# Optimization experiments

Hardware: AMD Instinct MI355X
Metric: run time of the kernel (lower is better)

## Reference

```python
import jax, jax.numpy as jnp
import numpy as np

I = 512
H = 512
B = 64
T = 512

def _lstm_step(W_ih, W_hh, b_ih, b_hh):
    def step(carry, xt):
        h, c = carry
        # gates in torch LSTMCell order: i, f, g, o
        gates = xt @ W_ih.T + b_ih + h @ W_hh.T + b_hh  # [B, 4H]
        i, f, g, o = jnp.split(gates, 4, axis=-1)
        c = jax.nn.sigmoid(f) * c + jax.nn.sigmoid(i) * jnp.tanh(g)
        h = jax.nn.sigmoid(o) * jnp.tanh(c)
        return (h, c), h
    return step

def setup_inputs() -> dict:
    key = jax.random.key(0)
    ks = jax.random.split(key, 9)
    s = 1.0 / np.sqrt(H)  # torch LSTMCell init: U(-1/sqrt(H), 1/sqrt(H))
    u = lambda k, shp: jax.random.uniform(k, shp, jnp.float32, -s, s)
    return {
        "xs": jax.random.normal(ks[0], (B, T, I), jnp.float32),
        "W_ih_f": u(ks[1], (4 * H, I)), "W_hh_f": u(ks[2], (4 * H, H)),
        "b_ih_f": u(ks[3], (4 * H,)), "b_hh_f": u(ks[4], (4 * H,)),
        "W_ih_b": u(ks[5], (4 * H, I)), "W_hh_b": u(ks[6], (4 * H, H)),
        "b_ih_b": u(ks[7], (4 * H,)), "b_hh_b": u(ks[8], (4 * H,)),
    }

def reference(xs, W_ih_f, W_hh_f, b_ih_f, b_hh_f, W_ih_b, W_hh_b, b_ih_b, b_hh_b):
    x = jnp.transpose(xs, (1, 0, 2))  # batch_first -> [T, B, I]
    b, h = x.shape[1], W_hh_f.shape[1]
    init = (jnp.zeros((b, h), x.dtype), jnp.zeros((b, h), x.dtype))
    _, hs_fwd = jax.lax.scan(_lstm_step(W_ih_f, W_hh_f, b_ih_f, b_hh_f), init, x)
    # reverse direction: scan backward, outputs land at original time indices
    _, hs_bwd = jax.lax.scan(_lstm_step(W_ih_b, W_hh_b, b_ih_b, b_hh_b), init, x, reverse=True)
    rst = jnp.concatenate([hs_fwd, hs_bwd], axis=-1)  # [T, B, 2H]
    return jnp.transpose(rst, (1, 0, 2))  # back to [B, T, 2H]
```

## Files before the change

### kernel.cpp

```cpp
#include <hip/hip_runtime.h>
#include <math.h>

#define B 64
#define T 512
#define II 512
#define H 512
#define NBLK 256

typedef float f32x4 __attribute__((ext_vector_type(4)));
typedef short s16x8 __attribute__((ext_vector_type(8)));
typedef unsigned u32;
typedef unsigned long long u64;

union pk8 { s16x8 v; u32 u[4]; };
union pk2 { u64 a[2]; uint4 q; };

__device__ __forceinline__ unsigned short f2b(float f){
  union { float f; u32 u; } v; v.f = f;
  u32 r = v.u + 0x7fffu + ((v.u >> 16) & 1u);
  return (unsigned short)(r >> 16);
}

__device__ __forceinline__ s16x8 cvt8(float4 lo, float4 hi){
  pk8 r;
  asm("v_cvt_pk_bf16_f32 %0, %1, %2" : "=v"(r.u[0]) : "v"(lo.x), "v"(lo.y));
  asm("v_cvt_pk_bf16_f32 %0, %1, %2" : "=v"(r.u[1]) : "v"(lo.z), "v"(lo.w));
  asm("v_cvt_pk_bf16_f32 %0, %1, %2" : "=v"(r.u[2]) : "v"(hi.x), "v"(hi.y));
  asm("v_cvt_pk_bf16_f32 %0, %1, %2" : "=v"(r.u[3]) : "v"(hi.z), "v"(hi.w));
  return r.v;
}

__device__ __forceinline__ float sigm_(float x){
  return __builtin_amdgcn_rcpf(1.f + __expf(-x));
}
__device__ __forceinline__ float tanh_(float x){
  float t = __expf(-2.f * fabsf(x));
  float r = (1.f - t) * __builtin_amdgcn_rcpf(1.f + t);
  return copysignf(r, x);
}

__global__ void init_ws(u32* p, int n){
  int i = blockIdx.x*blockDim.x + threadIdx.x;
  for (; i < n; i += gridDim.x*blockDim.x) p[i] = 0u;
}

__global__ __launch_bounds__(256, 1) void lstm_persistent(
    const float* __restrict__ xs,
    const float* __restrict__ Wih_f, const float* __restrict__ Whh_f,
    const float* __restrict__ bih_f, const float* __restrict__ bhh_f,
    const float* __restrict__ Wih_b, const float* __restrict__ Whh_b,
    const float* __restrict__ bih_b, const float* __restrict__ bhh_b,
    float* __restrict__ out,
    u32* __restrict__ flags,
    u32* __restrict__ hbuf0, u32* __restrict__ hbuf1)
{
  __shared__ unsigned short Wlds[4*16*1024];
  __shared__ unsigned short Hlds[16*512];
  __shared__ float g_lds[4][16][16];
  __shared__ float bias_s[64];

  const int tid = threadIdx.x;
  const int bx = blockIdx.x;
  const int dir   = bx >> 7;
  const int qtile = bx & 31;
  const int btile = (bx >> 5) & 3;
  const int grp   = bx >> 5;
  const int q0 = qtile * 16;
  const int b0 = btile * 16;

  const float* __restrict__ Wih = dir ? Wih_b : Wih_f;
  const float* __restrict__ Whh = dir ? Whh_b : Whh_f;
  const float* __restrict__ bih = dir ? bih_b : bih_f;
  const float* __restrict__ bhh = dir ? bhh_b : bhh_f;

  for (int it = 0; it < 32; ++it){
    int idx = it * 256 + tid;
    int c64 = idx >> 7;
    int k   = (idx & 127) * 8;
    int cg  = (c64 >> 4) * H + q0 + (c64 & 15);
    const float* src = (k < II) ? (Wih + (size_t)cg * II + k)
                                : (Whh + (size_t)cg * H + (k - II));
    float4 lo = *(const float4*)src;
    float4 hi = *(const float4*)(src + 4);
    s16x8 v;
    v[0]=(short)f2b(lo.x); v[1]=(short)f2b(lo.y); v[2]=(short)f2b(lo.z); v[3]=(short)f2b(lo.w);
    v[4]=(short)f2b(hi.x); v[5]=(short)f2b(hi.y); v[6]=(short)f2b(hi.z); v[7]=(short)f2b(hi.w);
    u32 byte = ((u32)c64 * 2048u + (u32)k * 2u) ^ (((u32)(c64 & 7)) << 4);
    *(s16x8*)((char*)Wlds + byte) = v;
  }
  if (tid < 64){
    int g = tid >> 4, jj = tid & 15;
    int cg = g * H + q0 + jj;
    bias_s[tid] = bih[cg] + bhh[cg];
  }
  __syncthreads();

  const int w = tid >> 6;
  const int l = tid & 63;
  const int arow = b0 + (l & 15);
  const int kgrp = (l >> 4) * 8;
  const int c64w = (w << 4) | (l & 15);
  const u32 swz   = ((u32)(c64w & 7)) << 4;
  const u32 wbase = (u32)c64w * 2048u;
  const u32 hrb = (u32)(l & 15) * 1024u;
  const u32 hsz = ((u32)(l & 7)) << 4;

  const int sr = w * 4;
  const int si = l;

  const int eb = tid >> 4;
  const int ej = tid & 15;
  float c_reg = 0.f;

  const size_t hdir = (size_t)dir * (B * (H/2));
  u32* const fl = flags + grp * 32;

  s16x8 a_x[16];
  {
    const int t0 = dir ? (T-1) : 0;
    const float* xrow = xs + ((size_t)arow * T + t0) * II + kgrp;
    #pragma unroll
    for (int ks = 0; ks < 16; ++ks)
      a_x[ks] = cvt8(*(const float4*)(xrow + ks*32), *(const float4*)(xrow + ks*32 + 4));
  }

  #pragma unroll 1
  for (int s = 0; s < T; ++s){
    const int t = dir ? (T - 1 - s) : s;
    const u32* __restrict__ hin  = (s & 1) ? hbuf1 : hbuf0;
    u32* __restrict__       hout = (s & 1) ? hbuf0 : hbuf1;

    if (s > 0){
      for (;;){
        u32 v = __hip_atomic_load(&fl[si & 31], __ATOMIC_RELAXED, __HIP_MEMORY_SCOPE_AGENT);
        if (__all((int)(v >= (u32)s))) break;
      }
    }

    u64 hv[8];
    #pragma unroll
    for (int p = 0; p < 4; ++p){
      const u64* src = (const u64*)(hin + hdir + (size_t)(b0 + sr + p) * (H/2)) + (size_t)si * 2;
      hv[2*p+0] = __hip_atomic_load(src + 0, __ATOMIC_RELAXED, __HIP_MEMORY_SCOPE_AGENT);
      hv[2*p+1] = __hip_atomic_load(src + 1, __ATOMIC_RELAXED, __HIP_MEMORY_SCOPE_AGENT);
    }

    f32x4 acc_xa = {0.f,0.f,0.f,0.f}, acc_xb = {0.f,0.f,0.f,0.f};
    #pragma unroll
    for (int ks = 0; ks < 8; ++ks){
      u32 byte0 = (wbase + (u32)(ks*32 + kgrp) * 2u) ^ swz;
      u32 byte1 = (wbase + (u32)((ks+8)*32 + kgrp) * 2u) ^ swz;
      s16x8 b0f = *(const s16x8*)((const char*)Wlds + byte0);
      s16x8 b1f = *(const s16x8*)((const char*)Wlds + byte1);
      acc_xa = __builtin_amdgcn_mfma_f32_16x16x32_bf16(a_x[ks],   b0f, acc_xa, 0, 0, 0);
      acc_xb = __builtin_amdgcn_mfma_f32_16x16x32_bf16(a_x[ks+8], b1f, acc_xb, 0, 0, 0);
    }

    #pragma unroll
    for (int p = 0; p < 4; ++p){
      int r = sr + p;
      u32 byte = ((u32)r * 1024u + (u32)si * 16u) ^ (((u32)(r & 7)) << 4);
      pk2 u; u.a[0] = hv[2*p+0]; u.a[1] = hv[2*p+1];
      *(uint4*)((char*)Hlds + byte) = u.q;
    }
    __syncthreads();

    f32x4 acc_ha = {0.f,0.f,0.f,0.f}, acc_hb = {0.f,0.f,0.f,0.f};
    #pragma unroll
    for (int ks = 0; ks < 8; ++ks){
      u32 hb0 = (hrb + (u32)(ks*64 + (kgrp*2))) ^ hsz;
      u32 hb1 = (hrb + (u32)((ks+8)*64 + (kgrp*2))) ^ hsz;
      s16x8 a0 = *(const s16x8*)((const char*)Hlds + hb0);
      s16x8 a1 = *(const s16x8*)((const char*)Hlds + hb1);
      u32 byte0 = (wbase + (u32)(II + ks*32 + kgrp) * 2u) ^ swz;
      u32 byte1 = (wbase + (u32)(II + (ks+8)*32 + kgrp) * 2u) ^ swz;
      s16x8 b0f = *(const s16x8*)((const char*)Wlds + byte0);
      s16x8 b1f = *(const s16x8*)((const char*)Wlds + byte1);
      acc_ha = __builtin_amdgcn_mfma_f32_16x16x32_bf16(a0, b0f, acc_ha, 0, 0, 0);
      acc_hb = __builtin_amdgcn_mfma_f32_16x16x32_bf16(a1, b1f, acc_hb, 0, 0, 0);
    }

    #pragma unroll
    for (int r = 0; r < 4; ++r){
      int bl = (l >> 4) * 4 + r;
      g_lds[w][bl][l & 15] = acc_xa[r] + acc_xb[r] + acc_ha[r] + acc_hb[r];
    }
    __syncthreads();

    float hn;
    {
      float gi = g_lds[0][eb][ej] + bias_s[ej];
      float gf = g_lds[1][eb][ej] + bias_s[16 + ej];
      float gg = g_lds[2][eb][ej] + bias_s[32 + ej];
      float go = g_lds[3][eb][ej] + bias_s[48 + ej];
      float si_ = sigm_(gi);
      float sf  = sigm_(gf);
      float tg  = tanh_(gg);
      float so  = sigm_(go);
      c_reg = sf * c_reg + si_ * tg;
      hn = so * tanh_(c_reg);
      u32 hb = (u32)f2b(hn);
      u32 nb = (u32)__shfl_xor((int)hb, 1, 64);
      if (!(tid & 1)){
        size_t idx = hdir + (size_t)(b0 + eb) * (H/2) + (size_t)((q0 + ej) >> 1);
        __hip_atomic_store(hout + idx, hb | (nb << 16),
                           __ATOMIC_RELAXED, __HIP_MEMORY_SCOPE_AGENT);
      }
    }

    __syncthreads();

    if (tid == 0 && s + 1 < T)
      __hip_atomic_store(&fl[qtile], (u32)(s + 1),
                         __ATOMIC_RELAXED, __HIP_MEMORY_SCOPE_AGENT);

    out[((size_t)(b0+eb) * T + t) * (2*H) + (size_t)dir * H + (q0 + ej)] = hn;
    if (s + 1 < T){
      const int tn = dir ? (T - 2 - s) : (s + 1);
      const float* xrow = xs + ((size_t)arow * T + tn) * II + kgrp;
      #pragma unroll
      for (int ks = 0; ks < 16; ++ks)
        a_x[ks] = cvt8(*(const float4*)(xrow + ks*32), *(const float4*)(xrow + ks*32 + 4));
    }
  }
}

extern "C" void kernel_launch(void* const* d_in, const int* in_sizes, int n_in,
                              void* d_out, int out_size, void* d_ws, size_t ws_size,
                              hipStream_t stream)
{
  const float* xs    = (const float*)d_in[0];
  const float* Wih_f = (const float*)d_in[1];
  const float* Whh_f = (const float*)d_in[2];
  const float* bih_f = (const float*)d_in[3];
  const float* bhh_f = (const float*)d_in[4];
  const float* Wih_b = (const float*)d_in[5];
  const float* Whh_b = (const float*)d_in[6];
  const float* bih_b = (const float*)d_in[7];
  const float* bhh_b = (const float*)d_in[8];
  float* out = (float*)d_out;

  char* ws = (char*)d_ws;
  u32* flags = (u32*)ws;
  u32* hbuf0 = (u32*)(ws + 4096);
  u32* hbuf1 = (u32*)(ws + 4096 + 2*B*(H/2)*4);

  const int init_u32 = (4096 + 2*(2*B*(H/2)*4)) / 4;
  init_ws<<<128, 256, 0, stream>>>((u32*)ws, init_u32);

  lstm_persistent<<<NBLK, 256, 0, stream>>>(
      xs, Wih_f, Whh_f, bih_f, bhh_f,
      Wih_b, Whh_b, bih_b, bhh_b,
      out, flags, hbuf0, hbuf1);
}
```

Baseline: 2.672 ms.

## Assign block roles by XCC so each recurrence group syncs within one L2

```diff
diff --git a/kernel.cpp b/kernel.cpp
--- a/kernel.cpp
+++ b/kernel.cpp
@@ -13,7 +13,6 @@
 typedef unsigned long long u64;
 
 union pk8 { s16x8 v; u32 u[4]; };
-union pk2 { u64 a[2]; uint4 q; };
 
 __device__ __forceinline__ unsigned short f2b(float f){
   union { float f; u32 u; } v; v.f = f;
@@ -39,9 +38,32 @@
   return copysignf(r, x);
 }
 
+__device__ __forceinline__ u32 ld_sc0_u32(const u32* p){
+  u32 v;
+  asm volatile("global_load_dword %0, %1, off sc0\n\ts_waitcnt vmcnt(0)"
+               : "=v"(v) : "v"(p) : "memory");
+  return v;
+}
+__device__ __forceinline__ void st_sc0_u32(u32* p, u32 v){
+  asm volatile("global_store_dword %0, %1, off sc0" : : "v"(p), "v"(v) : "memory");
+}
+__device__ __forceinline__ void ld4_sc0_issue(const void* p0, const void* p1,
+                                              const void* p2, const void* p3,
+                                              uint4& a, uint4& b, uint4& c, uint4& d){
+  asm volatile(
+    "global_load_dwordx4 %0, %4, off sc0\n\t"
+    "global_load_dwordx4 %1, %5, off sc0\n\t"
+    "global_load_dwordx4 %2, %6, off sc0\n\t"
+    "global_load_dwordx4 %3, %7, off sc0"
+    : "=&v"(a), "=&v"(b), "=&v"(c), "=&v"(d)
+    : "v"(p0), "v"(p1), "v"(p2), "v"(p3)
+    : "memory");
+}
+
 __global__ void init_ws(u32* p, int n){
   int i = blockIdx.x*blockDim.x + threadIdx.x;
-  for (; i < n; i += gridDim.x*blockDim.x) p[i] = 0u;
+  for (; i < n; i += gridDim.x*blockDim.x)
+    __hip_atomic_store(p + i, 0u, __ATOMIC_RELAXED, __HIP_MEMORY_SCOPE_AGENT);
 }
 
 __global__ __launch_bounds__(256, 1) void lstm_persistent(
@@ -52,19 +74,31 @@
     const float* __restrict__ bih_b, const float* __restrict__ bhh_b,
     float* __restrict__ out,
     u32* __restrict__ flags,
+    u32* __restrict__ roster,
     u32* __restrict__ hbuf0, u32* __restrict__ hbuf1)
 {
   __shared__ unsigned short Wlds[4*16*1024];
   __shared__ unsigned short Hlds[16*512];
   __shared__ float g_lds[4][16][16];
   __shared__ float bias_s[64];
+  __shared__ u32 role_s;
 
   const int tid = threadIdx.x;
-  const int bx = blockIdx.x;
-  const int dir   = bx >> 7;
-  const int qtile = bx & 31;
-  const int btile = (bx >> 5) & 3;
-  const int grp   = bx >> 5;
+
+  if (tid == 0){
+    u32 xcc;
+    asm volatile("s_getreg_b32 %0, hwreg(HW_REG_XCC_ID, 0, 32)" : "=s"(xcc));
+    xcc &= 7u;
+    u32 slot = __hip_atomic_fetch_add(&roster[xcc], 1u,
+                                      __ATOMIC_RELAXED, __HIP_MEMORY_SCOPE_AGENT);
+    role_s = (xcc << 5) | (slot & 31u);
+  }
+  __syncthreads();
+  const u32 role = role_s;
+  const int grp   = role >> 5;
+  const int qtile = role & 31;
+  const int dir   = grp >> 2;
+  const int btile = grp & 3;
   const int q0 = qtile * 16;
   const int b0 = btile * 16;
 
@@ -131,19 +165,21 @@
     u32* __restrict__       hout = (s & 1) ? hbuf0 : hbuf1;
 
     if (s > 0){
+      const u32* fp = fl + (l & 31);
       for (;;){
-        u32 v = __hip_atomic_load(&fl[si & 31], __ATOMIC_RELAXED, __HIP_MEMORY_SCOPE_AGENT);
+        u32 v = ld_sc0_u32(fp);
         if (__all((int)(v >= (u32)s))) break;
+        __builtin_amdgcn_s_sleep(1);
       }
     }
 
-    u64 hv[8];
-    #pragma unroll
-    for (int p = 0; p < 4; ++p){
-      const u64* src = (const u64*)(hin + hdir + (size_t)(b0 + sr + p) * (H/2)) + (size_t)si * 2;
-      hv[2*p+0] = __hip_atomic_load(src + 0, __ATOMIC_RELAXED, __HIP_MEMORY_SCOPE_AGENT);
-      hv[2*p+1] = __hip_atomic_load(src + 1, __ATOMIC_RELAXED, __HIP_MEMORY_SCOPE_AGENT);
-    }
+    const char* hinb = (const char*)(hin + hdir);
+    const char* r0p = hinb + (size_t)(b0 + sr + 0) * 1024 + (size_t)si * 16;
+    const char* r1p = r0p + 1024;
+    const char* r2p = r0p + 2048;
+    const char* r3p = r0p + 3072;
+    uint4 hva, hvb, hvc, hvd;
+    ld4_sc0_issue(r0p, r1p, r2p, r3p, hva, hvb, hvc, hvd);
 
     f32x4 acc_xa = {0.f,0.f,0.f,0.f}, acc_xb = {0.f,0.f,0.f,0.f};
     #pragma unroll
@@ -156,12 +192,17 @@
       acc_xb = __builtin_amdgcn_mfma_f32_16x16x32_bf16(a_x[ks+8], b1f, acc_xb, 0, 0, 0);
     }
 
-    #pragma unroll
-    for (int p = 0; p < 4; ++p){
-      int r = sr + p;
-      u32 byte = ((u32)r * 1024u + (u32)si * 16u) ^ (((u32)(r & 7)) << 4);
-      pk2 u; u.a[0] = hv[2*p+0]; u.a[1] = hv[2*p+1];
-      *(uint4*)((char*)Hlds + byte) = u.q;
+    asm volatile("s_waitcnt vmcnt(0)" ::: "memory");
+    __builtin_amdgcn_sched_barrier(0);
+    {
+      u32 byte0 = ((u32)(sr+0) * 1024u + (u32)si * 16u) ^ (((u32)((sr+0) & 7)) << 4);
+      u32 byte1 = ((u32)(sr+1) * 1024u + (u32)si * 16u) ^ (((u32)((sr+1) & 7)) << 4);
+      u32 byte2 = ((u32)(sr+2) * 1024u + (u32)si * 16u) ^ (((u32)((sr+2) & 7)) << 4);
+      u32 byte3 = ((u32)(sr+3) * 1024u + (u32)si * 16u) ^ (((u32)((sr+3) & 7)) << 4);
+      *(uint4*)((char*)Hlds + byte0) = hva;
+      *(uint4*)((char*)Hlds + byte1) = hvb;
+      *(uint4*)((char*)Hlds + byte2) = hvc;
+      *(uint4*)((char*)Hlds + byte3) = hvd;
     }
     __syncthreads();
 
@@ -202,17 +243,15 @@
       u32 hb = (u32)f2b(hn);
       u32 nb = (u32)__shfl_xor((int)hb, 1, 64);
       if (!(tid & 1)){
-        size_t idx = hdir + (size_t)(b0 + eb) * (H/2) + (size_t)((q0 + ej) >> 1);
-        __hip_atomic_store(hout + idx, hb | (nb << 16),
-                           __ATOMIC_RELAXED, __HIP_MEMORY_SCOPE_AGENT);
+        u32* p = hout + hdir + (size_t)(b0 + eb) * (H/2) + (size_t)((q0 + ej) >> 1);
+        st_sc0_u32(p, hb | (nb << 16));
       }
     }
 
+    asm volatile("s_waitcnt vmcnt(0)" ::: "memory");
     __syncthreads();
-
     if (tid == 0 && s + 1 < T)
-      __hip_atomic_store(&fl[qtile], (u32)(s + 1),
-                         __ATOMIC_RELAXED, __HIP_MEMORY_SCOPE_AGENT);
+      st_sc0_u32(&fl[qtile], (u32)(s + 1));
 
     out[((size_t)(b0+eb) * T + t) * (2*H) + (size_t)dir * H + (q0 + ej)] = hn;
     if (s + 1 < T){
@@ -241,9 +280,10 @@
   float* out = (float*)d_out;
 
   char* ws = (char*)d_ws;
-  u32* flags = (u32*)ws;
-  u32* hbuf0 = (u32*)(ws + 4096);
-  u32* hbuf1 = (u32*)(ws + 4096 + 2*B*(H/2)*4);
+  u32* flags  = (u32*)ws;
+  u32* roster = (u32*)(ws + 2048);
+  u32* hbuf0  = (u32*)(ws + 4096);
+  u32* hbuf1  = (u32*)(ws + 4096 + 2*B*(H/2)*4);
 
   const int init_u32 = (4096 + 2*(2*B*(H/2)*4)) / 4;
   init_ws<<<128, 256, 0, stream>>>((u32*)ws, init_u32);
@@ -251,5 +291,5 @@
   lstm_persistent<<<NBLK, 256, 0, stream>>>(
       xs, Wih_f, Whh_f, bih_f, bhh_f,
       Wih_b, Whh_b, bih_b, bhh_b,
-      out, flags, hbuf0, hbuf1);
-}
+      out, flags, roster, hbuf0, hbuf1);
+}
```

After: 2.616 ms. 2.1% less time.
